# Optimization experiments

Measured on AMD Instinct MI355X. Metric: run time of the kernel, lower is better.

The kernel has to match this reference:

```python
import jax, jax.numpy as jnp
import numpy as np
import math

D_MODEL, N_HEADS, D_K, D_V = 512, 2, 64, 64
C_CLIP = 10.0
MASK_FILL = -10.0

def setup_inputs() -> dict:
    key = jax.random.key(0)
    ks = jax.random.split(key, 12)
    B, Lq, Lk = 4, 2048, 2048
    s = 1.0 / math.sqrt(D_MODEL)
    return {
        "Q": jax.random.normal(ks[0], (B, Lq, D_MODEL), jnp.float32),
        "K": jax.random.normal(ks[1], (B, Lk, D_MODEL), jnp.float32),
        "V": jax.random.normal(ks[2], (B, Lk, D_MODEL), jnp.float32),
        "mask": jax.random.randint(ks[3], (B, Lk), 0, 2) > 0,
        "Wq": jax.random.normal(ks[4], (D_MODEL, N_HEADS * D_K), jnp.float32) * s,
        "bq": jnp.zeros((N_HEADS * D_K,), jnp.float32),
        "Wk": jax.random.normal(ks[5], (D_MODEL, N_HEADS * D_K), jnp.float32) * s,
        "bk": jnp.zeros((N_HEADS * D_K,), jnp.float32),
        "Wv": jax.random.normal(ks[6], (D_MODEL, N_HEADS * D_V), jnp.float32) * s,
        "bv": jnp.zeros((N_HEADS * D_V,), jnp.float32),
        "Wo": jax.random.normal(ks[7], (N_HEADS * D_V, D_MODEL), jnp.float32) * s,
        "bo": jnp.zeros((D_MODEL,), jnp.float32),
    }

def reference(Q, K, V, mask, Wq, bq, Wk, bk, Wv, bv, Wo, bo):
    B, Lq, _ = Q.shape
    Lk = K.shape[1]
    # project and split heads: [B, h, L, d]
    q = (Q @ Wq + bq).reshape(B, Lq, N_HEADS, D_K).transpose(0, 2, 1, 3)
    k = (K @ Wk + bk).reshape(B, Lk, N_HEADS, D_K).transpose(0, 2, 1, 3)
    v = (V @ Wv + bv).reshape(B, Lk, N_HEADS, D_V).transpose(0, 2, 1, 3)
    scores = jnp.einsum("bhqd,bhkd->bhqk", q, k) / jnp.sqrt(jnp.float32(D_K))
    scores = jnp.tanh(scores) * C_CLIP
    scores = jnp.where(mask[:, None, None, :], MASK_FILL, scores)
    attn = jax.nn.log_softmax(scores, axis=-1)  # NOTE: log-softmax used directly as weights
    out = jnp.einsum("bhqk,bhkd->bhqd", attn, v)
    out = out.transpose(0, 2, 1, 3).reshape(B, Lq, N_HEADS * D_V)
    out = out @ Wo + bo
    return (out, attn)
```

## Files before the change

kernel.cpp:

```cpp
#include <hip/hip_runtime.h>

typedef __attribute__((ext_vector_type(8))) short short8;
typedef __attribute__((ext_vector_type(4))) short short4v;
typedef __attribute__((ext_vector_type(4))) float f32x4;

#define DEVI static __device__ __forceinline__

constexpr int NB   = 4;
constexpr int NH   = 2;
constexpr int SEQ  = 2048;
constexpr int DM   = 512;
constexpr int DKV  = 64;
constexpr int HDIM = 128;

DEVI unsigned short f2bf(float f) {
    union { float f; unsigned u; } v; v.f = f;
    unsigned r = v.u + 0x7FFFu + ((v.u >> 16) & 1u);
    return (unsigned short)(r >> 16);
}
DEVI float bf2f(unsigned short s) {
    union { unsigned u; float f; } v; v.u = ((unsigned)s) << 16; return v.f;
}
DEVI unsigned pk2(float a, float b) {
    return (unsigned)f2bf(a) | ((unsigned)f2bf(b) << 16);
}
DEVI void async16(const void* g, void* l) {
    __builtin_amdgcn_global_load_lds(
        (const __attribute__((address_space(1))) unsigned int*)g,
        (__attribute__((address_space(3))) unsigned int*)l, 16, 0, 0);
}

__global__ __launch_bounds__(256) void k_prep(
    const float* __restrict__ Wq, const float* __restrict__ Wk,
    const float* __restrict__ Wv, const float* __restrict__ Wo,
    unsigned short* __restrict__ Wqt, unsigned short* __restrict__ Wkt,
    unsigned short* __restrict__ Wvt, unsigned short* __restrict__ Wot) {
    __shared__ unsigned short T[64][72];
    const int bid = blockIdx.x, tid = threadIdx.x;
    const float* src; unsigned short* dst; int ss, ds, k0, n0;
    if (bid < 48) {
        int m = bid >> 4, t16 = bid & 15;
        src = m == 0 ? Wq : (m == 1 ? Wk : Wv);
        dst = m == 0 ? Wqt : (m == 1 ? Wkt : Wvt);
        ss = 128; ds = 512;
        k0 = (t16 >> 1) * 64; n0 = (t16 & 1) * 64;
    } else {
        int t16 = bid - 48;
        src = Wo; dst = Wot; ss = 512; ds = 128;
        k0 = (t16 >> 3) * 64; n0 = (t16 & 7) * 64;
    }
    const int kk = tid >> 4, nn4 = (tid & 15) * 4;
    #pragma unroll
    for (int i = 0; i < 4; ++i) {
        float4 v = *(const float4*)(src + (size_t)(k0 + kk + i * 16) * ss + n0 + nn4);
        T[kk + i * 16][nn4]     = f2bf(v.x);
        T[kk + i * 16][nn4 + 1] = f2bf(v.y);
        T[kk + i * 16][nn4 + 2] = f2bf(v.z);
        T[kk + i * 16][nn4 + 3] = f2bf(v.w);
    }
    __syncthreads();
    const int nn = tid >> 2, kc = (tid & 3) * 16;
    unsigned short tmp[16];
    #pragma unroll
    for (int i = 0; i < 16; ++i) tmp[i] = T[kc + i][nn];
    unsigned short* o = dst + (size_t)(n0 + nn) * ds + k0 + kc;
    *(uint4*)o       = *(uint4*)tmp;
    *(uint4*)(o + 8) = *(uint4*)(tmp + 8);
}

__global__ __launch_bounds__(256) void k_proj(
    const float* __restrict__ Qg, const float* __restrict__ Kg, const float* __restrict__ Vg,
    const unsigned short* __restrict__ Wqt, const unsigned short* __restrict__ Wkt,
    const unsigned short* __restrict__ Wvt,
    const float* __restrict__ bq, const float* __restrict__ bk, const float* __restrict__ bv,
    unsigned short* __restrict__ qs, unsigned short* __restrict__ kb,
    unsigned short* __restrict__ vt) {
    __shared__ unsigned short lA[64 * 64];
    __shared__ unsigned short lB[128 * 64];

    const int y = blockIdx.y;
    const float* X = y == 0 ? Qg : (y == 1 ? Kg : Vg);
    const unsigned short* Wt = y == 0 ? Wqt : (y == 1 ? Wkt : Wvt);
    const float* bias = y == 0 ? bq : (y == 1 ? bk : bv);
    const float scal = y == 0 ? 0.125f : 1.0f;
    const int row0 = blockIdx.x * 64;
    const int tid = threadIdx.x, lane = tid & 63, wv = tid >> 6;
    const int l16 = lane & 15, lq4 = lane >> 4;
    const int wr = wv >> 1, wc = wv & 1;

    f32x4 acc[2][4];
    #pragma unroll
    for (int i = 0; i < 2; ++i)
        #pragma unroll
        for (int j = 0; j < 4; ++j) acc[i][j] = f32x4{0.f, 0.f, 0.f, 0.f};

    const int arow = tid >> 2, ac0 = (tid & 3) * 16;

    for (int kc = 0; kc < 8; ++kc) {
        {
            const float* src = X + (size_t)(row0 + arow) * DM + kc * 64 + ac0;
            unsigned short* dst = &lA[arow * 64 + ac0];
            #pragma unroll
            for (int i = 0; i < 4; ++i) {
                float4 v = *(const float4*)(src + 4 * i);
                unsigned p0 = (unsigned)f2bf(v.x) | ((unsigned)f2bf(v.y) << 16);
                unsigned p1 = (unsigned)f2bf(v.z) | ((unsigned)f2bf(v.w) << 16);
                *(unsigned*)(dst + 4 * i) = p0;
                *(unsigned*)(dst + 4 * i + 2) = p1;
            }
        }
        #pragma unroll
        for (int c = 0; c < 4; ++c) {
            int chunk = wv * 4 + c;
            int n = chunk * 8 + (lane >> 3);
            int kpart = (lane & 7) * 8;
            const void* g = (const char*)Wt + ((size_t)n * DM + kc * 64 + kpart) * 2;
            void* l = (char*)lB + chunk * 1024 + lane * 16;
            async16(g, l);
        }
        __syncthreads();

        #pragma unroll
        for (int ks = 0; ks < 2; ++ks) {
            short8 a[2], b[4];
            #pragma unroll
            for (int mt = 0; mt < 2; ++mt) {
                int m = wr * 32 + mt * 16 + l16;
                a[mt] = *(const short8*)&lA[m * 64 + ks * 32 + lq4 * 8];
            }
            #pragma unroll
            for (int nt = 0; nt < 4; ++nt) {
                int n = wc * 64 + nt * 16 + l16;
                b[nt] = *(const short8*)&lB[n * 64 + ks * 32 + lq4 * 8];
            }
            #pragma unroll
            for (int mt = 0; mt < 2; ++mt)
                #pragma unroll
                for (int nt = 0; nt < 4; ++nt)
                    acc[mt][nt] = __builtin_amdgcn_mfma_f32_16x16x32_bf16(
                        a[mt], b[nt], acc[mt][nt], 0, 0, 0);
        }
        __syncthreads();
    }

    if (y < 2) {
        unsigned short* dstp = (y == 0) ? qs : kb;
        #pragma unroll
        for (int mt = 0; mt < 2; ++mt)
            #pragma unroll
            for (int nt = 0; nt < 4; ++nt) {
                int col = wc * 64 + nt * 16 + l16;
                float bb = bias[col];
                int h = col >> 6, d = col & 63;
                #pragma unroll
                for (int r = 0; r < 4; ++r) {
                    int row = row0 + wr * 32 + mt * 16 + lq4 * 4 + r;
                    int b = row >> 11, pos = row & 2047;
                    float val = (acc[mt][nt][r] + bb) * scal;
                    dstp[((size_t)(b * NH + h) * SEQ + pos) * DKV + d] = f2bf(val);
                }
            }
    } else {
        #pragma unroll
        for (int mt = 0; mt < 2; ++mt)
            #pragma unroll
            for (int nt = 0; nt < 4; ++nt) {
                int col = wc * 64 + nt * 16 + l16;
                float bb = bias[col];
                #pragma unroll
                for (int r = 0; r < 4; ++r) {
                    int mrow = wr * 32 + mt * 16 + lq4 * 4 + r;
                    lB[col * 64 + mrow] = f2bf(acc[mt][nt][r] + bb);
                }
            }
        __syncthreads();
        int c = tid >> 1, mp = (tid & 1) * 32;
        int b = row0 >> 11, kpos0 = row0 & 2047;
        int h = c >> 6, d = c & 63;
        unsigned short* dst = vt + ((size_t)(b * NH + h) * DKV + d) * SEQ + kpos0 + mp;
        const unsigned short* srcl = &lB[c * 64 + mp];
        #pragma unroll
        for (int i = 0; i < 4; ++i)
            *(uint4*)(dst + 8 * i) = *(const uint4*)(srcl + 8 * i);
    }
}

__global__ __launch_bounds__(256) void k_pass1(
    const unsigned short* __restrict__ qs, const unsigned short* __restrict__ kb,
    const int* __restrict__ maskg, float* __restrict__ Lpart) {
    __shared__ float lsumW[4 * 64];

    const int bx = blockIdx.x;
    const int bh = bx & 7;
    const int qt = (bx >> 3) & 31;
    const int ksp = bx >> 8;
    const int qbase = qt * 64;
    const int b = bh >> 1;
    const int tid = threadIdx.x, lane = tid & 63, wv = tid >> 6;
    const int l16 = lane & 15, lq4 = lane >> 4;

    short8 aq[4][2];
    #pragma unroll
    for (int mt = 0; mt < 4; ++mt)
        #pragma unroll
        for (int ks = 0; ks < 2; ++ks) {
            size_t off = ((size_t)bh * SEQ + qbase + mt * 16 + l16) * DKV + ks * 32 + lq4 * 8;
            aq[mt][ks] = *(const short8*)(qs + off);
        }

    float sums[4][4];
    #pragma unroll
    for (int mt = 0; mt < 4; ++mt)
        #pragma unroll
        for (int r = 0; r < 4; ++r) sums[mt][r] = 0.f;

    const unsigned short* kB = kb + (size_t)bh * SEQ * DKV;
    const int* mB = maskg + b * SEQ;

    #pragma unroll 2
    for (int kt = 0; kt < 4; ++kt) {
        const int kbase = ksp * 512 + kt * 128;
        short8 bfr[2][2];
        int mv[2];
        #pragma unroll
        for (int nt = 0; nt < 2; ++nt) {
            int n = kbase + wv * 32 + nt * 16 + l16;
            const unsigned short* p = kB + (size_t)n * DKV + lq4 * 8;
            bfr[0][nt] = *(const short8*)p;
            bfr[1][nt] = *(const short8*)(p + 32);
            mv[nt] = mB[n];
        }

        f32x4 acc[4][2];
        #pragma unroll
        for (int mt = 0; mt < 4; ++mt)
            #pragma unroll
            for (int nt = 0; nt < 2; ++nt) acc[mt][nt] = f32x4{0.f, 0.f, 0.f, 0.f};
        #pragma unroll
        for (int ks = 0; ks < 2; ++ks)
            #pragma unroll
            for (int mt = 0; mt < 4; ++mt)
                #pragma unroll
                for (int nt = 0; nt < 2; ++nt)
                    acc[mt][nt] = __builtin_amdgcn_mfma_f32_16x16x32_bf16(
                        aq[mt][ks], bfr[ks][nt], acc[mt][nt], 0, 0, 0);

        #pragma unroll
        for (int nt = 0; nt < 2; ++nt) {
            int m_ = mv[nt];
            #pragma unroll
            for (int mt = 0; mt < 4; ++mt)
                #pragma unroll
                for (int r = 0; r < 4; ++r) {
                    float x = acc[mt][nt][r];
                    float e2 = __expf(2.f * x);
                    float s10 = 10.f - 20.f * __builtin_amdgcn_rcpf(1.f + e2);
                    float s = m_ ? -10.f : s10;
                    sums[mt][r] += __expf(s);
                }
        }
    }

    #pragma unroll
    for (int mt = 0; mt < 4; ++mt)
        #pragma unroll
        for (int r = 0; r < 4; ++r) {
            float v = sums[mt][r];
            v += __shfl_xor(v, 1); v += __shfl_xor(v, 2);
            v += __shfl_xor(v, 4); v += __shfl_xor(v, 8);
            if (l16 == 0) lsumW[wv * 64 + mt * 16 + lq4 * 4 + r] = v;
        }
    __syncthreads();
    if (tid < 64) {
        float v = lsumW[tid] + lsumW[64 + tid] + lsumW[128 + tid] + lsumW[192 + tid];
        Lpart[(size_t)ksp * (8 * SEQ) + (size_t)bh * SEQ + qbase + tid] = v;
    }
}

__global__ __launch_bounds__(256) void k_pass2(
    const unsigned short* __restrict__ qs, const unsigned short* __restrict__ kb,
    const unsigned short* __restrict__ vt, const int* __restrict__ maskg,
    const float* __restrict__ Lpart, float* __restrict__ attnG, float* __restrict__ outh2) {
    __shared__ unsigned short lV[64 * 128];
    __shared__ unsigned short lAttn[64 * 136];

    const int bx = blockIdx.x;
    const int bh = bx & 7;
    const int qt = (bx >> 3) & 31;
    const int ksp = bx >> 8;
    const int qbase = qt * 64;
    const int b = bh >> 1, h = bh & 1;
    const int tid = threadIdx.x, lane = tid & 63, wv = tid >> 6;
    const int l16 = lane & 15, lq4 = lane >> 4;

    short8 aq[4][2];
    #pragma unroll
    for (int mt = 0; mt < 4; ++mt)
        #pragma unroll
        for (int ks = 0; ks < 2; ++ks) {
            size_t off = ((size_t)bh * SEQ + qbase + mt * 16 + l16) * DKV + ks * 32 + lq4 * 8;
            aq[mt][ks] = *(const short8*)(qs + off);
        }

    float Lr[4][4];
    #pragma unroll
    for (int mt = 0; mt < 4; ++mt)
        #pragma unroll
        for (int r = 0; r < 4; ++r) {
            size_t idx = (size_t)bh * SEQ + qbase + mt * 16 + lq4 * 4 + r;
            float s = Lpart[idx] + Lpart[8 * SEQ + idx] +
                      Lpart[2 * 8 * SEQ + idx] + Lpart[3 * 8 * SEQ + idx];
            Lr[mt][r] = __logf(s);
        }

    f32x4 o[4];
    #pragma unroll
    for (int mt = 0; mt < 4; ++mt) o[mt] = f32x4{0.f, 0.f, 0.f, 0.f};

    const unsigned short* kB = kb + (size_t)bh * SEQ * DKV;
    const int* mB = maskg + b * SEQ;

    for (int kt = 0; kt < 4; ++kt) {
        const int kbase = ksp * 512 + kt * 128;

        #pragma unroll
        for (int c = 0; c < 4; ++c) {
            int chunk = wv * 4 + c;
            int d = chunk * 4 + (lane >> 4);
            int kk = (lane & 15) * 8;
            const void* g = (const char*)vt + (((size_t)bh * DKV + d) * SEQ + kbase + kk) * 2;
            void* l = (char*)lV + chunk * 1024 + lane * 16;
            async16(g, l);
        }

        short8 bfr[2][2];
        int mv[2];
        #pragma unroll
        for (int nt = 0; nt < 2; ++nt) {
            int n = kbase + wv * 32 + nt * 16 + l16;
            const unsigned short* p = kB + (size_t)n * DKV + lq4 * 8;
            bfr[0][nt] = *(const short8*)p;
            bfr[1][nt] = *(const short8*)(p + 32);
            mv[nt] = mB[n];
        }
        f32x4 s[4][2];
        #pragma unroll
        for (int mt = 0; mt < 4; ++mt)
            #pragma unroll
            for (int nt = 0; nt < 2; ++nt) s[mt][nt] = f32x4{0.f, 0.f, 0.f, 0.f};
        #pragma unroll
        for (int ks = 0; ks < 2; ++ks)
            #pragma unroll
            for (int mt = 0; mt < 4; ++mt)
                #pragma unroll
                for (int nt = 0; nt < 2; ++nt)
                    s[mt][nt] = __builtin_amdgcn_mfma_f32_16x16x32_bf16(
                        aq[mt][ks], bfr[ks][nt], s[mt][nt], 0, 0, 0);

        #pragma unroll
        for (int nt = 0; nt < 2; ++nt) {
            int col = wv * 32 + nt * 16 + l16;
            int m_ = mv[nt];
            #pragma unroll
            for (int mt = 0; mt < 4; ++mt)
                #pragma unroll
                for (int r = 0; r < 4; ++r) {
                    float x = s[mt][nt][r];
                    float e2 = __expf(2.f * x);
                    float s10 = 10.f - 20.f * __builtin_amdgcn_rcpf(1.f + e2);
                    float a = (m_ ? -10.f : s10) - Lr[mt][r];
                    lAttn[(mt * 16 + lq4 * 4 + r) * 136 + col] = f2bf(a);
                }
        }
        __syncthreads();

        #pragma unroll
        for (int ks = 0; ks < 4; ++ks) {
            short8 bfr2 = *(const short8*)&lV[(wv * 16 + l16) * 128 + ks * 32 + lq4 * 8];
            #pragma unroll
            for (int mt = 0; mt < 4; ++mt) {
                short8 af = *(const short8*)&lAttn[(mt * 16 + l16) * 136 + ks * 32 + lq4 * 8];
                o[mt] = __builtin_amdgcn_mfma_f32_16x16x32_bf16(af, bfr2, o[mt], 0, 0, 0);
            }
        }
        #pragma unroll
        for (int j = 0; j < 8; ++j) {
            int row = j * 8 + (tid >> 5);
            int col = (tid & 31) * 4;
            short4v hv = *(const short4v*)&lAttn[row * 136 + col];
            float4 f;
            f.x = bf2f((unsigned short)hv[0]); f.y = bf2f((unsigned short)hv[1]);
            f.z = bf2f((unsigned short)hv[2]); f.w = bf2f((unsigned short)hv[3]);
            float* gdst = attnG + ((size_t)bh * SEQ + qbase + row) * SEQ + kbase + col;
            *(float4*)gdst = f;
        }
        __syncthreads();
    }

    float* dst = outh2 + (size_t)ksp * (8192 * HDIM);
    #pragma unroll
    for (int mt = 0; mt < 4; ++mt)
        #pragma unroll
        for (int r = 0; r < 4; ++r) {
            int q = qbase + mt * 16 + lq4 * 4 + r;
            int dcol = wv * 16 + l16;
            dst[((size_t)b * SEQ + q) * HDIM + h * DKV + dcol] = o[mt][r];
        }
}

__global__ __launch_bounds__(256) void k_oproj(
    const float* __restrict__ outh2, const unsigned short* __restrict__ Wot,
    const float* __restrict__ bo, float* __restrict__ outG) {
    __shared__ unsigned short lA2[128 * 128];
    __shared__ unsigned short lB2[128 * 128];
    const int row0 = blockIdx.x * 128, col0 = blockIdx.y * 128;
    const int tid = threadIdx.x, lane = tid & 63, wv = tid >> 6;
    const int l16 = lane & 15, lq4 = lane >> 4;
    const int wr = wv >> 1, wc = wv & 1;

    #pragma unroll
    for (int c = 0; c < 8; ++c) {
        int chunk = wv * 8 + c;
        int row = chunk * 4 + (lane >> 4);
        int gslot = (lane & 15) ^ (row & 7);
        async16((const char*)Wot + ((size_t)(col0 + row)) * 256 + gslot * 16,
                (char*)lB2 + chunk * 1024 + lane * 16);
    }
    {
        const int c16 = tid & 31;
        const int rb = tid >> 5;
        #pragma unroll
        for (int i = 0; i < 16; ++i) {
            int r = rb + i * 8;
            size_t off = (size_t)(row0 + r) * 128 + c16 * 4;
            float4 a = *(const float4*)(outh2 + off);
            float4 b = *(const float4*)(outh2 + 1048576 + off);
            float4 c = *(const float4*)(outh2 + 2 * 1048576 + off);
            float4 d = *(const float4*)(outh2 + 3 * 1048576 + off);
            unsigned p0 = pk2(a.x + b.x + c.x + d.x, a.y + b.y + c.y + d.y);
            unsigned p1 = pk2(a.z + b.z + c.z + d.z, a.w + b.w + c.w + d.w);
            unsigned long long pk =
                (unsigned long long)p0 | ((unsigned long long)p1 << 32);
            unsigned bo2 = (unsigned)(r * 256 + c16 * 8) ^ ((unsigned)(r & 7) << 4);
            *(unsigned long long*)((char*)lA2 + bo2) = pk;
        }
    }
    __syncthreads();

    f32x4 acc[4][4];
    #pragma unroll
    for (int mt = 0; mt < 4; ++mt)
        #pragma unroll
        for (int nt = 0; nt < 4; ++nt) acc[mt][nt] = f32x4{0.f, 0.f, 0.f, 0.f};

    #pragma unroll
    for (int ks = 0; ks < 4; ++ks) {
        short8 a[4], bfr[4];
        #pragma unroll
        for (int mt = 0; mt < 4; ++mt) {
            int m = wr * 64 + mt * 16 + l16;
            unsigned ao = (unsigned)(m * 256 + ks * 64 + lq4 * 16) ^ ((unsigned)(m & 7) << 4);
            a[mt] = *(const short8*)((const char*)lA2 + ao);
        }
        #pragma unroll
        for (int nt = 0; nt < 4; ++nt) {
            int n = wc * 64 + nt * 16 + l16;
            unsigned bo2 = (unsigned)(n * 256 + ks * 64 + lq4 * 16) ^ ((unsigned)(n & 7) << 4);
            bfr[nt] = *(const short8*)((const char*)lB2 + bo2);
        }
        #pragma unroll
        for (int mt = 0; mt < 4; ++mt)
            #pragma unroll
            for (int nt = 0; nt < 4; ++nt)
                acc[mt][nt] = __builtin_amdgcn_mfma_f32_16x16x32_bf16(
                    a[mt], bfr[nt], acc[mt][nt], 0, 0, 0);
    }

    #pragma unroll
    for (int nt = 0; nt < 4; ++nt) {
        int col = col0 + wc * 64 + nt * 16 + l16;
        float bb = bo[col];
        #pragma unroll
        for (int mt = 0; mt < 4; ++mt)
            #pragma unroll
            for (int r = 0; r < 4; ++r) {
                int row = row0 + wr * 64 + mt * 16 + lq4 * 4 + r;
                outG[(size_t)row * DM + col] = acc[mt][nt][r] + bb;
            }
    }
}

extern "C" void kernel_launch(void* const* d_in, const int* in_sizes, int n_in,
                              void* d_out, int out_size, void* d_ws, size_t ws_size,
                              hipStream_t stream) {
    (void)in_sizes; (void)n_in; (void)out_size; (void)ws_size;
    const float* Qg = (const float*)d_in[0];
    const float* Kg = (const float*)d_in[1];
    const float* Vg = (const float*)d_in[2];
    const int*   maskg = (const int*)d_in[3];
    const float* Wq = (const float*)d_in[4];
    const float* bq = (const float*)d_in[5];
    const float* Wk = (const float*)d_in[6];
    const float* bk = (const float*)d_in[7];
    const float* Wv = (const float*)d_in[8];
    const float* bv = (const float*)d_in[9];
    const float* Wo = (const float*)d_in[10];
    const float* bo = (const float*)d_in[11];

    char* ws = (char*)d_ws;
    unsigned short* qs   = (unsigned short*)(ws);
    unsigned short* kb   = (unsigned short*)(ws + (4  << 20));
    unsigned short* vt   = (unsigned short*)(ws + (8  << 20));
    float*          outh2= (float*)(ws + (12 << 20));
    float*          Lpart= (float*)(ws + (30 << 20));
    unsigned short* Wqt  = (unsigned short*)(ws + (30 << 20) + 262144);
    unsigned short* Wkt  = (unsigned short*)((char*)Wqt + 131072);
    unsigned short* Wvt  = (unsigned short*)((char*)Wkt + 131072);
    unsigned short* Wot  = (unsigned short*)((char*)Wvt + 131072);

    float* outG  = (float*)d_out;
    float* attnG = outG + (size_t)NB * SEQ * DM;

    hipLaunchKernelGGL(k_prep, dim3(64), dim3(256), 0, stream,
                       Wq, Wk, Wv, Wo, Wqt, Wkt, Wvt, Wot);
    hipLaunchKernelGGL(k_proj, dim3(128, 3), dim3(256), 0, stream,
                       Qg, Kg, Vg, Wqt, Wkt, Wvt, bq, bk, bv, qs, kb, vt);
    hipLaunchKernelGGL(k_pass1, dim3(1024), dim3(256), 0, stream, qs, kb, maskg, Lpart);
    hipLaunchKernelGGL(k_pass2, dim3(1024), dim3(256), 0, stream,
                       qs, kb, vt, maskg, Lpart, attnG, outh2);
    hipLaunchKernelGGL(k_oproj, dim3(64, 4), dim3(256), 0, stream, outh2, Wot, bo, outG);
}
```

Measured before the change: 261.5 us.

## Fuse score-sum and PV passes, defer log-normalizer via V column sums

The separate normalizer pass is merged into the attention kernel. It now multiplies raw clipped scores by V, stores the raw scores as bf16 in a scratch buffer, and accumulates the exp-sums and per-head V column sums. A new finalize kernel subtracts log(sum) from the bf16 scores and writes the fp32 attention matrix. The output projection corrects the PV result with -L*sum(V). This removes one full QK^T and tanh recompute pass, but adds a bf16 write and read of the 4x2x2048x2048 score matrix and an extra launch.

```diff
diff --git a/kernel.cpp b/kernel.cpp
--- a/kernel.cpp
+++ b/kernel.cpp
@@ -185,104 +185,14 @@
     }
 }
 
-__global__ __launch_bounds__(256) void k_pass1(
-    const unsigned short* __restrict__ qs, const unsigned short* __restrict__ kb,
-    const int* __restrict__ maskg, float* __restrict__ Lpart) {
-    __shared__ float lsumW[4 * 64];
-
-    const int bx = blockIdx.x;
-    const int bh = bx & 7;
-    const int qt = (bx >> 3) & 31;
-    const int ksp = bx >> 8;
-    const int qbase = qt * 64;
-    const int b = bh >> 1;
-    const int tid = threadIdx.x, lane = tid & 63, wv = tid >> 6;
-    const int l16 = lane & 15, lq4 = lane >> 4;
-
-    short8 aq[4][2];
-    #pragma unroll
-    for (int mt = 0; mt < 4; ++mt)
-        #pragma unroll
-        for (int ks = 0; ks < 2; ++ks) {
-            size_t off = ((size_t)bh * SEQ + qbase + mt * 16 + l16) * DKV + ks * 32 + lq4 * 8;
-            aq[mt][ks] = *(const short8*)(qs + off);
-        }
-
-    float sums[4][4];
-    #pragma unroll
-    for (int mt = 0; mt < 4; ++mt)
-        #pragma unroll
-        for (int r = 0; r < 4; ++r) sums[mt][r] = 0.f;
-
-    const unsigned short* kB = kb + (size_t)bh * SEQ * DKV;
-    const int* mB = maskg + b * SEQ;
-
-    #pragma unroll 2
-    for (int kt = 0; kt < 4; ++kt) {
-        const int kbase = ksp * 512 + kt * 128;
-        short8 bfr[2][2];
-        int mv[2];
-        #pragma unroll
-        for (int nt = 0; nt < 2; ++nt) {
-            int n = kbase + wv * 32 + nt * 16 + l16;
-            const unsigned short* p = kB + (size_t)n * DKV + lq4 * 8;
-            bfr[0][nt] = *(const short8*)p;
-            bfr[1][nt] = *(const short8*)(p + 32);
-            mv[nt] = mB[n];
-        }
-
-        f32x4 acc[4][2];
-        #pragma unroll
-        for (int mt = 0; mt < 4; ++mt)
-            #pragma unroll
-            for (int nt = 0; nt < 2; ++nt) acc[mt][nt] = f32x4{0.f, 0.f, 0.f, 0.f};
-        #pragma unroll
-        for (int ks = 0; ks < 2; ++ks)
-            #pragma unroll
-            for (int mt = 0; mt < 4; ++mt)
-                #pragma unroll
-                for (int nt = 0; nt < 2; ++nt)
-                    acc[mt][nt] = __builtin_amdgcn_mfma_f32_16x16x32_bf16(
-                        aq[mt][ks], bfr[ks][nt], acc[mt][nt], 0, 0, 0);
-
-        #pragma unroll
-        for (int nt = 0; nt < 2; ++nt) {
-            int m_ = mv[nt];
-            #pragma unroll
-            for (int mt = 0; mt < 4; ++mt)
-                #pragma unroll
-                for (int r = 0; r < 4; ++r) {
-                    float x = acc[mt][nt][r];
-                    float e2 = __expf(2.f * x);
-                    float s10 = 10.f - 20.f * __builtin_amdgcn_rcpf(1.f + e2);
-                    float s = m_ ? -10.f : s10;
-                    sums[mt][r] += __expf(s);
-                }
-        }
-    }
-
-    #pragma unroll
-    for (int mt = 0; mt < 4; ++mt)
-        #pragma unroll
-        for (int r = 0; r < 4; ++r) {
-            float v = sums[mt][r];
-            v += __shfl_xor(v, 1); v += __shfl_xor(v, 2);
-            v += __shfl_xor(v, 4); v += __shfl_xor(v, 8);
-            if (l16 == 0) lsumW[wv * 64 + mt * 16 + lq4 * 4 + r] = v;
-        }
-    __syncthreads();
-    if (tid < 64) {
-        float v = lsumW[tid] + lsumW[64 + tid] + lsumW[128 + tid] + lsumW[192 + tid];
-        Lpart[(size_t)ksp * (8 * SEQ) + (size_t)bh * SEQ + qbase + tid] = v;
-    }
-}
-
-__global__ __launch_bounds__(256) void k_pass2(
+__global__ __launch_bounds__(256) void k_attn(
     const unsigned short* __restrict__ qs, const unsigned short* __restrict__ kb,
     const unsigned short* __restrict__ vt, const int* __restrict__ maskg,
-    const float* __restrict__ Lpart, float* __restrict__ attnG, float* __restrict__ outh2) {
+    unsigned short* __restrict__ sg, float* __restrict__ Lpart,
+    float* __restrict__ vsumPart, float* __restrict__ outh2) {
     __shared__ unsigned short lV[64 * 128];
     __shared__ unsigned short lAttn[64 * 136];
+    __shared__ float lsumW[4 * 64];
 
     const int bx = blockIdx.x;
     const int bh = bx & 7;
@@ -302,20 +212,17 @@
             aq[mt][ks] = *(const short8*)(qs + off);
         }
 
-    float Lr[4][4];
+    float sums[4][4];
     #pragma unroll
     for (int mt = 0; mt < 4; ++mt)
         #pragma unroll
-        for (int r = 0; r < 4; ++r) {
-            size_t idx = (size_t)bh * SEQ + qbase + mt * 16 + lq4 * 4 + r;
-            float s = Lpart[idx] + Lpart[8 * SEQ + idx] +
-                      Lpart[2 * 8 * SEQ + idx] + Lpart[3 * 8 * SEQ + idx];
-            Lr[mt][r] = __logf(s);
-        }
+        for (int r = 0; r < 4; ++r) sums[mt][r] = 0.f;
 
     f32x4 o[4];
     #pragma unroll
     for (int mt = 0; mt < 4; ++mt) o[mt] = f32x4{0.f, 0.f, 0.f, 0.f};
+
+    float vsum_acc = 0.f;
 
     const unsigned short* kB = kb + (size_t)bh * SEQ * DKV;
     const int* mB = maskg + b * SEQ;
@@ -368,8 +275,9 @@
                     float x = s[mt][nt][r];
                     float e2 = __expf(2.f * x);
                     float s10 = 10.f - 20.f * __builtin_amdgcn_rcpf(1.f + e2);
-                    float a = (m_ ? -10.f : s10) - Lr[mt][r];
-                    lAttn[(mt * 16 + lq4 * 4 + r) * 136 + col] = f2bf(a);
+                    float sraw = m_ ? -10.f : s10;
+                    sums[mt][r] += __expf(sraw);
+                    lAttn[(mt * 16 + lq4 * 4 + r) * 136 + col] = f2bf(sraw);
                 }
         }
         __syncthreads();
@@ -384,17 +292,45 @@
             }
         }
         #pragma unroll
-        for (int j = 0; j < 8; ++j) {
-            int row = j * 8 + (tid >> 5);
-            int col = (tid & 31) * 4;
-            short4v hv = *(const short4v*)&lAttn[row * 136 + col];
-            float4 f;
-            f.x = bf2f((unsigned short)hv[0]); f.y = bf2f((unsigned short)hv[1]);
-            f.z = bf2f((unsigned short)hv[2]); f.w = bf2f((unsigned short)hv[3]);
-            float* gdst = attnG + ((size_t)bh * SEQ + qbase + row) * SEQ + kbase + col;
-            *(float4*)gdst = f;
+        for (int j = 0; j < 4; ++j) {
+            int row = j * 16 + (tid >> 4);
+            int col = (tid & 15) * 8;
+            *(short8*)(sg + ((size_t)bh * SEQ + qbase + row) * SEQ + kbase + col) =
+                *(const short8*)&lAttn[row * 136 + col];
+        }
+        if (qt == 0) {
+            int d = tid >> 2, k0 = (tid & 3) * 32;
+            float a = 0.f;
+            #pragma unroll
+            for (int i = 0; i < 4; ++i) {
+                short8 vv = *(const short8*)&lV[d * 128 + k0 + i * 8];
+                #pragma unroll
+                for (int t = 0; t < 8; ++t) a += bf2f((unsigned short)vv[t]);
+            }
+            vsum_acc += a;
         }
         __syncthreads();
+    }
+
+    #pragma unroll
+    for (int mt = 0; mt < 4; ++mt)
+        #pragma unroll
+        for (int r = 0; r < 4; ++r) {
+            float v = sums[mt][r];
+            v += __shfl_xor(v, 1); v += __shfl_xor(v, 2);
+            v += __shfl_xor(v, 4); v += __shfl_xor(v, 8);
+            if (l16 == 0) lsumW[wv * 64 + mt * 16 + lq4 * 4 + r] = v;
+        }
+    __syncthreads();
+    if (tid < 64) {
+        float v = lsumW[tid] + lsumW[64 + tid] + lsumW[128 + tid] + lsumW[192 + tid];
+        Lpart[(size_t)ksp * (8 * SEQ) + (size_t)bh * SEQ + qbase + tid] = v;
+    }
+
+    if (qt == 0) {
+        float v = vsum_acc;
+        v += __shfl_xor(v, 1); v += __shfl_xor(v, 2);
+        if ((tid & 3) == 0) vsumPart[ksp * 512 + bh * 64 + (tid >> 2)] = v;
     }
 
     float* dst = outh2 + (size_t)ksp * (8192 * HDIM);
@@ -408,9 +344,42 @@
         }
 }
 
+__global__ __launch_bounds__(256) void k_fin(
+    const unsigned short* __restrict__ sg, const float* __restrict__ Lpart,
+    float* __restrict__ attnG) {
+    const int bx = blockIdx.x;
+    const int bh = bx & 7;
+    const int q0 = (bx >> 3) * 16;
+    const int tid = threadIdx.x;
+    const int row = tid >> 4;
+    const size_t ridx = (size_t)bh * SEQ + q0 + row;
+    const float Lv = __logf(Lpart[ridx] + Lpart[16384 + ridx] +
+                            Lpart[32768 + ridx] + Lpart[49152 + ridx]);
+    const unsigned short* srow = sg + ridx * SEQ;
+    float* drow = attnG + ridx * SEQ;
+    const int c0 = (tid & 15) * 8;
+    #pragma unroll
+    for (int j = 0; j < 16; ++j) {
+        int c = j * 128 + c0;
+        short8 v = *(const short8*)(srow + c);
+        float4 fa, fb;
+        fa.x = bf2f((unsigned short)v[0]) - Lv;
+        fa.y = bf2f((unsigned short)v[1]) - Lv;
+        fa.z = bf2f((unsigned short)v[2]) - Lv;
+        fa.w = bf2f((unsigned short)v[3]) - Lv;
+        fb.x = bf2f((unsigned short)v[4]) - Lv;
+        fb.y = bf2f((unsigned short)v[5]) - Lv;
+        fb.z = bf2f((unsigned short)v[6]) - Lv;
+        fb.w = bf2f((unsigned short)v[7]) - Lv;
+        *(float4*)(drow + c) = fa;
+        *(float4*)(drow + c + 4) = fb;
+    }
+}
+
 __global__ __launch_bounds__(256) void k_oproj(
     const float* __restrict__ outh2, const unsigned short* __restrict__ Wot,
-    const float* __restrict__ bo, float* __restrict__ outG) {
+    const float* __restrict__ bo, const float* __restrict__ Lpart,
+    const float* __restrict__ vsumPart, float* __restrict__ outG) {
     __shared__ unsigned short lA2[128 * 128];
     __shared__ unsigned short lB2[128 * 128];
     const int row0 = blockIdx.x * 128, col0 = blockIdx.y * 128;
@@ -429,21 +398,56 @@
     {
         const int c16 = tid & 31;
         const int rb = tid >> 5;
+        const int hcol = (c16 * 4) >> 6;
+        const int d0 = (c16 * 4) & 63;
+        float4 vs;
+        {
+            float4 v0 = *(const float4*)(vsumPart + hcol * 64 + d0);
+            float4 v1 = *(const float4*)(vsumPart + 512 + hcol * 64 + d0);
+            float4 v2 = *(const float4*)(vsumPart + 1024 + hcol * 64 + d0);
+            float4 v3 = *(const float4*)(vsumPart + 1536 + hcol * 64 + d0);
+            vs.x = v0.x + v1.x + v2.x + v3.x;
+            vs.y = v0.y + v1.y + v2.y + v3.y;
+            vs.z = v0.z + v1.z + v2.z + v3.z;
+            vs.w = v0.w + v1.w + v2.w + v3.w;
+        }
         #pragma unroll
         for (int i = 0; i < 16; ++i) {
             int r = rb + i * 8;
-            size_t off = (size_t)(row0 + r) * 128 + c16 * 4;
+            int grow = row0 + r;
+            int b_ = grow >> 11, q = grow & 2047;
+            int bh = b_ * 2 + hcol;
+            float4 vsb;
+            {
+                float4 v0 = *(const float4*)(vsumPart + bh * 64 + d0);
+                float4 v1 = *(const float4*)(vsumPart + 512 + bh * 64 + d0);
+                float4 v2 = *(const float4*)(vsumPart + 1024 + bh * 64 + d0);
+                float4 v3 = *(const float4*)(vsumPart + 1536 + bh * 64 + d0);
+                vsb.x = v0.x + v1.x + v2.x + v3.x;
+                vsb.y = v0.y + v1.y + v2.y + v3.y;
+                vsb.z = v0.z + v1.z + v2.z + v3.z;
+                vsb.w = v0.w + v1.w + v2.w + v3.w;
+            }
+            size_t ridx = (size_t)bh * SEQ + q;
+            float Lv = __logf(Lpart[ridx] + Lpart[16384 + ridx] +
+                              Lpart[32768 + ridx] + Lpart[49152 + ridx]);
+            size_t off = (size_t)grow * 128 + c16 * 4;
             float4 a = *(const float4*)(outh2 + off);
             float4 b = *(const float4*)(outh2 + 1048576 + off);
             float4 c = *(const float4*)(outh2 + 2 * 1048576 + off);
             float4 d = *(const float4*)(outh2 + 3 * 1048576 + off);
-            unsigned p0 = pk2(a.x + b.x + c.x + d.x, a.y + b.y + c.y + d.y);
-            unsigned p1 = pk2(a.z + b.z + c.z + d.z, a.w + b.w + c.w + d.w);
+            float sx = a.x + b.x + c.x + d.x - Lv * vsb.x;
+            float sy = a.y + b.y + c.y + d.y - Lv * vsb.y;
+            float sz = a.z + b.z + c.z + d.z - Lv * vsb.z;
+            float sw = a.w + b.w + c.w + d.w - Lv * vsb.w;
+            unsigned p0 = pk2(sx, sy);
+            unsigned p1 = pk2(sz, sw);
             unsigned long long pk =
                 (unsigned long long)p0 | ((unsigned long long)p1 << 32);
             unsigned bo2 = (unsigned)(r * 256 + c16 * 8) ^ ((unsigned)(r & 7) << 4);
             *(unsigned long long*)((char*)lA2 + bo2) = pk;
         }
+        (void)vs;
     }
     __syncthreads();
 
@@ -508,15 +512,17 @@
     const float* bo = (const float*)d_in[11];
 
     char* ws = (char*)d_ws;
-    unsigned short* qs   = (unsigned short*)(ws);
-    unsigned short* kb   = (unsigned short*)(ws + (4  << 20));
-    unsigned short* vt   = (unsigned short*)(ws + (8  << 20));
-    float*          outh2= (float*)(ws + (12 << 20));
-    float*          Lpart= (float*)(ws + (30 << 20));
-    unsigned short* Wqt  = (unsigned short*)(ws + (30 << 20) + 262144);
-    unsigned short* Wkt  = (unsigned short*)((char*)Wqt + 131072);
-    unsigned short* Wvt  = (unsigned short*)((char*)Wkt + 131072);
-    unsigned short* Wot  = (unsigned short*)((char*)Wvt + 131072);
+    unsigned short* qs    = (unsigned short*)(ws);
+    unsigned short* kb    = (unsigned short*)(ws + (4  << 20));
+    unsigned short* vt    = (unsigned short*)(ws + (8  << 20));
+    float*          outh2 = (float*)(ws + (12 << 20));
+    float*          Lpart = (float*)(ws + (28 << 20));
+    float*          vsumP = (float*)(ws + (28 << 20) + 262144);
+    unsigned short* Wqt   = (unsigned short*)(ws + (29 << 20));
+    unsigned short* Wkt   = (unsigned short*)((char*)Wqt + 131072);
+    unsigned short* Wvt   = (unsigned short*)((char*)Wkt + 131072);
+    unsigned short* Wot   = (unsigned short*)((char*)Wvt + 131072);
+    unsigned short* sg    = (unsigned short*)(ws + ((size_t)32 << 20));
 
     float* outG  = (float*)d_out;
     float* attnG = outG + (size_t)NB * SEQ * DM;
@@ -525,8 +531,9 @@
                        Wq, Wk, Wv, Wo, Wqt, Wkt, Wvt, Wot);
     hipLaunchKernelGGL(k_proj, dim3(128, 3), dim3(256), 0, stream,
                        Qg, Kg, Vg, Wqt, Wkt, Wvt, bq, bk, bv, qs, kb, vt);
-    hipLaunchKernelGGL(k_pass1, dim3(1024), dim3(256), 0, stream, qs, kb, maskg, Lpart);
-    hipLaunchKernelGGL(k_pass2, dim3(1024), dim3(256), 0, stream,
-                       qs, kb, vt, maskg, Lpart, attnG, outh2);
-    hipLaunchKernelGGL(k_oproj, dim3(64, 4), dim3(256), 0, stream, outh2, Wot, bo, outG);
-}
+    hipLaunchKernelGGL(k_attn, dim3(1024), dim3(256), 0, stream,
+                       qs, kb, vt, maskg, sg, Lpart, vsumP, outh2);
+    hipLaunchKernelGGL(k_fin, dim3(1024), dim3(256), 0, stream, sg, Lpart, attnG);
+    hipLaunchKernelGGL(k_oproj, dim3(64, 4), dim3(256), 0, stream,
+                       outh2, Wot, bo, Lpart, vsumP, outG);
+}
```

New measurement: 300.6 us. +15.0%, slower.
